# Optimization experiments

Measured on AMD Instinct MI355X. Metric: run time of the kernel, lower is better.

Reference implementation:

```python
import jax, jax.numpy as jnp
import numpy as np


def setup_inputs() -> dict:
    key = jax.random.key(0)
    k1, k2 = jax.random.split(key)
    B, N, M = 4, 8192, 8192
    xyz1 = jax.random.normal(k1, (B, N, 3), dtype=jnp.float32)
    xyz2 = jax.random.normal(k2, (B, M, 3), dtype=jnp.float32)
    return {"xyz1": xyz1, "xyz2": xyz2}


def _chamfer(xyz1, xyz2):
    sq1 = jnp.sum(xyz1 * xyz1, axis=-1)  # [B, N]
    sq2 = jnp.sum(xyz2 * xyz2, axis=-1)  # [B, M]
    inner = jnp.einsum("bnc,bmc->bnm", xyz1, xyz2)  # [B, N, M]
    d = sq1[:, :, None] + sq2[:, None, :] - 2.0 * inner
    dist1 = jnp.min(d, axis=2)  # [B, N] nearest in xyz2 for each xyz1 point
    dist2 = jnp.min(d, axis=1)  # [B, M] nearest in xyz1 for each xyz2 point
    return dist1, dist2


def reference(xyz1, xyz2):
    return _chamfer(xyz1, xyz2)
```

## Files before the change

kernel.cpp:

```cpp
#include <hip/hip_runtime.h>

typedef _Float16 half8 __attribute__((ext_vector_type(8)));
typedef float f32x16 __attribute__((ext_vector_type(16)));

#define NQ 4
#define TS 4
#define GPW 16

__device__ __forceinline__ float min3f(float a, float b, float c) {
    float d;
    asm("v_min3_f32 %0, %1, %2, %3" : "=v"(d) : "v"(a), "v"(b), "v"(c));
    return d;
}

__global__ void cd_prep(const float* __restrict__ xyz1,
                        const float* __restrict__ xyz2,
                        _Float16* __restrict__ frag) {
    int tid  = blockIdx.x * 256 + threadIdx.x;
    int aidx = tid >> 14;
    int rem  = tid & 16383;
    int g = rem >> 6, l = rem & 63;
    int dir = aidx >> 2, b = aidx & 3;
    const float* src = (dir ? xyz1 : xyz2) + (size_t)b * 8192 * 3;
    int t = g * 32 + (l & 31);
    float x = src[t*3+0], y = src[t*3+1], z = src[t*3+2];
    float sq = __builtin_fmaf(x, x, __builtin_fmaf(y, y, z * z));
    _Float16 xh = (_Float16)x, yh = (_Float16)y, zh = (_Float16)z;
    _Float16 xl = (_Float16)(x - (float)xh);
    _Float16 yl = (_Float16)(y - (float)yh);
    _Float16 zl = (_Float16)(z - (float)zh);
    _Float16 sh = (_Float16)sq;
    _Float16 sl = (_Float16)(sq - (float)sh);
    const _Float16 one = (_Float16)1.0f, zero = (_Float16)0.0f;
    half8 f;
    if ((l >> 5) == 0) {
        f[0]=xh; f[1]=xh; f[2]=xl; f[3]=yh; f[4]=yh; f[5]=yl; f[6]=zh; f[7]=zh;
    } else {
        f[0]=zl; f[1]=sh; f[2]=sl; f[3]=one; f[4]=one; f[5]=zero; f[6]=zero; f[7]=zero;
    }
    ((half8*)frag)[(size_t)aidx * 16384 + g * 64 + l] = f;
}

#define FOLD8(Dv, acc)                                  \
    acc[0] = min3f(Dv[0],  Dv[1],  acc[0]);             \
    acc[1] = min3f(Dv[2],  Dv[3],  acc[1]);             \
    acc[2] = min3f(Dv[4],  Dv[5],  acc[2]);             \
    acc[3] = min3f(Dv[6],  Dv[7],  acc[3]);             \
    acc[4] = min3f(Dv[8],  Dv[9],  acc[4]);             \
    acc[5] = min3f(Dv[10], Dv[11], acc[5]);             \
    acc[6] = min3f(Dv[12], Dv[13], acc[6]);             \
    acc[7] = min3f(Dv[14], Dv[15], acc[7]);

__global__ void __launch_bounds__(256) cd_main(
        const float* __restrict__ xyz1, const float* __restrict__ xyz2,
        const _Float16* __restrict__ frag, unsigned int* __restrict__ out) {
    __shared__ float red[4][128];
    const int ts  = blockIdx.x;
    const int qt  = blockIdx.y;
    const int bd  = blockIdx.z;
    const int dir = bd >> 2, b = bd & 3;
    const int l = threadIdx.x & 63, w = threadIdx.x >> 6;
    const int h = l >> 5;
    const float* q = (dir ? xyz2 : xyz1) + (size_t)b * 8192 * 3;
    const int qbase = qt * 128;

    half8 Bf[NQ];
    const _Float16 one = (_Float16)1.0f, zero = (_Float16)0.0f;
    #pragma unroll
    for (int j = 0; j < NQ; ++j) {
        int qi = qbase + j * 32 + (l & 31);
        float px = q[qi*3+0], py = q[qi*3+1], pz = q[qi*3+2];
        float mx = -2.f * px, my = -2.f * py, mz = -2.f * pz;
        float sq = __builtin_fmaf(px, px, __builtin_fmaf(py, py, pz * pz));
        _Float16 mxh = (_Float16)mx, mxl = (_Float16)(mx - (float)mxh);
        _Float16 myh = (_Float16)my, myl = (_Float16)(my - (float)myh);
        _Float16 mzh = (_Float16)mz, mzl = (_Float16)(mz - (float)mzh);
        _Float16 sh  = (_Float16)sq, sl  = (_Float16)(sq - (float)sh);
        half8 f;
        if (h == 0) { f[0]=mxh; f[1]=mxl; f[2]=mxh; f[3]=myh; f[4]=myl; f[5]=myh; f[6]=mzh; f[7]=mzl; }
        else        { f[0]=mzh; f[1]=one; f[2]=one; f[3]=sh; f[4]=sl; f[5]=zero; f[6]=zero; f[7]=zero; }
        Bf[j] = f;
    }

    f32x16 Z;
    #pragma unroll
    for (int i = 0; i < 16; ++i) Z[i] = 0.f;

    float b8[NQ][8];
    #pragma unroll
    for (int j = 0; j < NQ; ++j)
        #pragma unroll
        for (int p = 0; p < 8; ++p) b8[j][p] = 3.0e38f;

    const half8* Ap = ((const half8*)frag) + (size_t)bd * 16384
                      + ((size_t)ts * 64 + (size_t)w * GPW) * 64 + l;

    half8 buf0 = Ap[0];
    half8 buf1 = Ap[64];
    #pragma unroll
    for (int g = 0; g < GPW; ++g) {
        half8 a = (g & 1) ? buf1 : buf0;
        if (g + 2 < GPW) {
            if (g & 1) buf1 = Ap[(size_t)(g + 2) * 64];
            else       buf0 = Ap[(size_t)(g + 2) * 64];
        }
        #pragma unroll
        for (int j = 0; j < NQ; ++j) {
            f32x16 D = __builtin_amdgcn_mfma_f32_32x32x16_f16(a, Bf[j], Z, 0, 0, 0);
            FOLD8(D, b8[j]);
        }
    }

    float best[NQ];
    #pragma unroll
    for (int j = 0; j < NQ; ++j) {
        float m01 = fminf(b8[j][0], b8[j][1]);
        float m23 = fminf(b8[j][2], b8[j][3]);
        float m45 = fminf(b8[j][4], b8[j][5]);
        float m67 = fminf(b8[j][6], b8[j][7]);
        best[j] = fminf(fminf(m01, m23), fminf(m45, m67));
    }

    #pragma unroll
    for (int j = 0; j < NQ; ++j) {
        float o = __shfl_xor(best[j], 32, 64);
        best[j] = fminf(best[j], o);
    }
    if (l < 32) {
        #pragma unroll
        for (int j = 0; j < NQ; ++j) red[w][j * 32 + l] = best[j];
    }
    __syncthreads();
    if (threadIdx.x < 128) {
        int t = threadIdx.x;
        float m = fminf(fminf(red[0][t], red[1][t]), fminf(red[2][t], red[3][t]));
        atomicMin(out + (size_t)dir * 32768 + (size_t)b * 8192 + qbase + t,
                  __float_as_uint(m));
    }
}

extern "C" void kernel_launch(void* const* d_in, const int* in_sizes, int n_in,
                              void* d_out, int out_size, void* d_ws, size_t ws_size,
                              hipStream_t stream) {
    const float* xyz1 = (const float*)d_in[0];
    const float* xyz2 = (const float*)d_in[1];
    _Float16* frag = (_Float16*)d_ws;

    hipMemsetAsync(d_out, 0x7F, (size_t)out_size * sizeof(float), stream);

    cd_prep<<<512, 256, 0, stream>>>(xyz1, xyz2, frag);

    dim3 grid(TS, 64, 8);
    cd_main<<<grid, 256, 0, stream>>>(xyz1, xyz2, frag, (unsigned int*)d_out);
}
```

Measured before the change: 37.55 us.

## Fuse target fragment prep into main kernel and drop atomics and memset

Removes the separate prep kernel and memset by converting target points to split-fp16 MFMA fragments inline, and makes each block cover all targets so results are written directly instead of via atomicMin. This cuts launch overhead and workspace traffic. In exchange, each block redundantly recomputes the fragment conversion, the grid shrinks fourfold, and explicit load prefetching is removed.

```diff
diff --git a/kernel.cpp b/kernel.cpp
--- a/kernel.cpp
+++ b/kernel.cpp
@@ -3,42 +3,14 @@
 typedef _Float16 half8 __attribute__((ext_vector_type(8)));
 typedef float f32x16 __attribute__((ext_vector_type(16)));
 
+#define TPB 256
 #define NQ 4
-#define TS 4
-#define GPW 16
+#define GPW 64
 
 __device__ __forceinline__ float min3f(float a, float b, float c) {
     float d;
     asm("v_min3_f32 %0, %1, %2, %3" : "=v"(d) : "v"(a), "v"(b), "v"(c));
     return d;
-}
-
-__global__ void cd_prep(const float* __restrict__ xyz1,
-                        const float* __restrict__ xyz2,
-                        _Float16* __restrict__ frag) {
-    int tid  = blockIdx.x * 256 + threadIdx.x;
-    int aidx = tid >> 14;
-    int rem  = tid & 16383;
-    int g = rem >> 6, l = rem & 63;
-    int dir = aidx >> 2, b = aidx & 3;
-    const float* src = (dir ? xyz1 : xyz2) + (size_t)b * 8192 * 3;
-    int t = g * 32 + (l & 31);
-    float x = src[t*3+0], y = src[t*3+1], z = src[t*3+2];
-    float sq = __builtin_fmaf(x, x, __builtin_fmaf(y, y, z * z));
-    _Float16 xh = (_Float16)x, yh = (_Float16)y, zh = (_Float16)z;
-    _Float16 xl = (_Float16)(x - (float)xh);
-    _Float16 yl = (_Float16)(y - (float)yh);
-    _Float16 zl = (_Float16)(z - (float)zh);
-    _Float16 sh = (_Float16)sq;
-    _Float16 sl = (_Float16)(sq - (float)sh);
-    const _Float16 one = (_Float16)1.0f, zero = (_Float16)0.0f;
-    half8 f;
-    if ((l >> 5) == 0) {
-        f[0]=xh; f[1]=xh; f[2]=xl; f[3]=yh; f[4]=yh; f[5]=yl; f[6]=zh; f[7]=zh;
-    } else {
-        f[0]=zl; f[1]=sh; f[2]=sl; f[3]=one; f[4]=one; f[5]=zero; f[6]=zero; f[7]=zero;
-    }
-    ((half8*)frag)[(size_t)aidx * 16384 + g * 64 + l] = f;
 }
 
 #define FOLD8(Dv, acc)                                  \
@@ -51,24 +23,26 @@
     acc[6] = min3f(Dv[12], Dv[13], acc[6]);             \
     acc[7] = min3f(Dv[14], Dv[15], acc[7]);
 
-__global__ void __launch_bounds__(256) cd_main(
+__global__ void __launch_bounds__(TPB) cd_fused(
         const float* __restrict__ xyz1, const float* __restrict__ xyz2,
-        const _Float16* __restrict__ frag, unsigned int* __restrict__ out) {
+        float* __restrict__ out) {
     __shared__ float red[4][128];
-    const int ts  = blockIdx.x;
-    const int qt  = blockIdx.y;
-    const int bd  = blockIdx.z;
+    const int qt  = blockIdx.x;
+    const int bd  = blockIdx.y;
     const int dir = bd >> 2, b = bd & 3;
     const int l = threadIdx.x & 63, w = threadIdx.x >> 6;
     const int h = l >> 5;
+    const int r32 = l & 31;
     const float* q = (dir ? xyz2 : xyz1) + (size_t)b * 8192 * 3;
+    const float* t = (dir ? xyz1 : xyz2) + (size_t)b * 8192 * 3;
     const int qbase = qt * 128;
 
+    const _Float16 one = (_Float16)1.0f, zero = (_Float16)0.0f;
+
     half8 Bf[NQ];
-    const _Float16 one = (_Float16)1.0f, zero = (_Float16)0.0f;
     #pragma unroll
     for (int j = 0; j < NQ; ++j) {
-        int qi = qbase + j * 32 + (l & 31);
+        int qi = qbase + j * 32 + r32;
         float px = q[qi*3+0], py = q[qi*3+1], pz = q[qi*3+2];
         float mx = -2.f * px, my = -2.f * py, mz = -2.f * pz;
         float sq = __builtin_fmaf(px, px, __builtin_fmaf(py, py, pz * pz));
@@ -92,18 +66,23 @@
         #pragma unroll
         for (int p = 0; p < 8; ++p) b8[j][p] = 3.0e38f;
 
-    const half8* Ap = ((const half8*)frag) + (size_t)bd * 16384
-                      + ((size_t)ts * 64 + (size_t)w * GPW) * 64 + l;
+    const float* tw = t + ((size_t)(w * GPW) * 32 + r32) * 3;
+    #pragma unroll 2
+    for (int g = 0; g < GPW; ++g) {
+        const float* tp = tw + (size_t)g * 96;
+        float x = tp[0], y = tp[1], z = tp[2];
+        float sq = __builtin_fmaf(x, x, __builtin_fmaf(y, y, z * z));
+        _Float16 xh = (_Float16)x, xl = (_Float16)(x - (float)xh);
+        _Float16 yh = (_Float16)y, yl = (_Float16)(y - (float)yh);
+        _Float16 zh = (_Float16)z, zl = (_Float16)(z - (float)zh);
+        _Float16 sh = (_Float16)sq, sl = (_Float16)(sq - (float)sh);
+        half8 a;
+        if (h == 0) {
+            a[0]=xh; a[1]=xh; a[2]=xl; a[3]=yh; a[4]=yh; a[5]=yl; a[6]=zh; a[7]=zh;
+        } else {
+            a[0]=zl; a[1]=sh; a[2]=sl; a[3]=one; a[4]=one; a[5]=zero; a[6]=zero; a[7]=zero;
+        }
 
-    half8 buf0 = Ap[0];
-    half8 buf1 = Ap[64];
-    #pragma unroll
-    for (int g = 0; g < GPW; ++g) {
-        half8 a = (g & 1) ? buf1 : buf0;
-        if (g + 2 < GPW) {
-            if (g & 1) buf1 = Ap[(size_t)(g + 2) * 64];
-            else       buf0 = Ap[(size_t)(g + 2) * 64];
-        }
         #pragma unroll
         for (int j = 0; j < NQ; ++j) {
             f32x16 D = __builtin_amdgcn_mfma_f32_32x32x16_f16(a, Bf[j], Z, 0, 0, 0);
@@ -120,7 +99,6 @@
         float m67 = fminf(b8[j][6], b8[j][7]);
         best[j] = fminf(fminf(m01, m23), fminf(m45, m67));
     }
-
     #pragma unroll
     for (int j = 0; j < NQ; ++j) {
         float o = __shfl_xor(best[j], 32, 64);
@@ -132,10 +110,9 @@
     }
     __syncthreads();
     if (threadIdx.x < 128) {
-        int t = threadIdx.x;
-        float m = fminf(fminf(red[0][t], red[1][t]), fminf(red[2][t], red[3][t]));
-        atomicMin(out + (size_t)dir * 32768 + (size_t)b * 8192 + qbase + t,
-                  __float_as_uint(m));
+        int ti = threadIdx.x;
+        float m = fminf(fminf(red[0][ti], red[1][ti]), fminf(red[2][ti], red[3][ti]));
+        out[(size_t)dir * 32768 + (size_t)b * 8192 + qbase + ti] = m;
     }
 }
 
@@ -144,12 +121,7 @@
                               hipStream_t stream) {
     const float* xyz1 = (const float*)d_in[0];
     const float* xyz2 = (const float*)d_in[1];
-    _Float16* frag = (_Float16*)d_ws;
 
-    hipMemsetAsync(d_out, 0x7F, (size_t)out_size * sizeof(float), stream);
-
-    cd_prep<<<512, 256, 0, stream>>>(xyz1, xyz2, frag);
-
-    dim3 grid(TS, 64, 8);
-    cd_main<<<grid, 256, 0, stream>>>(xyz1, xyz2, frag, (unsigned int*)d_out);
+    dim3 grid(64, 8);
+    cd_fused<<<grid, TPB, 0, stream>>>(xyz1, xyz2, (float*)d_out);
 }
```

Measured after the change: 40.25 us. +7.2%, slower.
